# Kernel tuning notes

Measured on AMD Instinct MI355X. Metric: run time of the kernel, lower is better.

Reference implementation:

```python
import jax, jax.numpy as jnp
import numpy as np

N_NODES = 50000
N_EDGES = 1250000
D = 64
EPS = 1e-07


def setup_inputs() -> dict:
    key = jax.random.key(0)
    ks = jax.random.split(key, 10)
    return {
        "node_feats": jax.random.normal(ks[0], (N_NODES, D), jnp.float32),
        "emb0": jax.random.normal(ks[1], (8, D), jnp.float32),
        "emb1": jax.random.normal(ks[2], (4, D), jnp.float32),
        "W": jax.random.normal(ks[3], (D, D), jnp.float32) / np.sqrt(D),
        "b": jnp.zeros((D,), jnp.float32),
        "beta": jnp.ones((1,), jnp.float32),
        "scale": jnp.ones((1,), jnp.float32),
        "src": jax.random.randint(ks[4], (N_EDGES,), 0, N_NODES),
        "dst": jax.random.randint(ks[5], (N_EDGES,), 0, N_NODES),
        "edge_feat0": jax.random.randint(ks[6], (N_EDGES,), 0, 8),
        "edge_feat1": jax.random.randint(ks[7], (N_EDGES,), 0, 4),
    }


def reference(node_feats, emb0, emb1, W, b, beta, scale, src, dst, edge_feat0, edge_feat1):
    n = node_feats.shape[0]
    # edge embeddings summed over categorical feature types
    e = emb0[edge_feat0] + emb1[edge_feat1]              # [E, D]
    # u_add_e then relu + eps
    m = jnp.maximum(node_feats[src] + e, 0.0) + EPS      # [E, D]
    # edge softmax over edges sharing the same destination (per feature dim)
    logits = m * beta                                    # [E, D]
    mx = jax.ops.segment_max(logits, dst, num_segments=n)
    ex = jnp.exp(logits - mx[dst])
    denom = jax.ops.segment_sum(ex, dst, num_segments=n)
    a = ex / denom[dst]                                  # [E, D]
    # scatter-sum aggregation of m * a to destination nodes
    msg = jax.ops.segment_sum(m * a, dst, num_segments=n)  # [N, D]
    # MessageNorm: L2-normalize msg, rescale by ||node_feats|| * scale
    msg_unit = msg / jnp.maximum(
        jnp.linalg.norm(msg, axis=-1, keepdims=True), 1e-12)
    feats_norm = jnp.linalg.norm(node_feats, axis=-1, keepdims=True)
    msg = msg_unit * feats_norm * scale
    # residual + single-layer MLP
    feats = node_feats + msg
    return feats @ W + b
```

## Files before the change

kernel.cpp:

```cpp
#include <hip/hip_runtime.h>

#define NN 50000
#define NE 1250000
#define DD 64
#define KR 391
#define RSH 7
#define RCAP 4096
#define RCSH 12


__global__ __launch_bounds__(512) void k_part(
    const int4* __restrict__ src4, const int4* __restrict__ dst4,
    const int4* __restrict__ ef04, const int4* __restrict__ ef14,
    const float* __restrict__ W, float* __restrict__ Wt,
    int* __restrict__ rcur, unsigned* __restrict__ staging)
{
    __shared__ int hist[KR], rbase[KR], cur[KR];
    const int t  = threadIdx.x;
    const int gb = blockIdx.x;

    for (int i = t; i < KR; i += 512) { hist[i] = 0; cur[i] = 0; }
    if (gb == 0)
        for (int i = t; i < 4096; i += 512)
            Wt[(i & 63) * DD + (i >> 6)] = W[i];
    __syncthreads();

    unsigned pay[8];
    int rr[8];
#pragma unroll
    for (int u = 0; u < 8; ++u) rr[u] = -1;

#pragma unroll
    for (int g = 0; g < 2; ++g) {
        const int i4 = gb * 1024 + t + g * 512;
        if (i4 < NE / 4) {
            const int4 s  = src4[i4], d = dst4[i4];
            const int4 f0 = ef04[i4], f1 = ef14[i4];
            const int ds[4] = {d.x, d.y, d.z, d.w};
            const int ss[4] = {s.x, s.y, s.z, s.w};
            const int a0[4] = {f0.x, f0.y, f0.z, f0.w};
            const int a1[4] = {f1.x, f1.y, f1.z, f1.w};
#pragma unroll
            for (int u = 0; u < 4; ++u) {
                const int k = g * 4 + u;
                rr[k]  = ds[u] >> RSH;
                pay[k] = (unsigned)ss[u] | ((unsigned)(a1[u] * 8 + a0[u]) << 16)
                         | ((unsigned)(ds[u] & 127) << 21);
            }
        }
    }
#pragma unroll
    for (int u = 0; u < 8; ++u)
        if (rr[u] >= 0) atomicAdd(&hist[rr[u]], 1);
    __syncthreads();

    for (int i = t; i < KR; i += 512) {
        const int h = hist[i];
        if (h) rbase[i] = atomicAdd(&rcur[i], h);
    }
    __syncthreads();

#pragma unroll
    for (int u = 0; u < 8; ++u) {
        if (rr[u] >= 0) {
            const int r   = rr[u];
            const int pos = rbase[r] + atomicAdd(&cur[r], 1);
            if (pos < RCAP) staging[(r << RCSH) + pos] = pay[u];
        }
    }
}

__global__ __launch_bounds__(256) void k_bucket(
    const unsigned* __restrict__ staging, const int* __restrict__ rcur,
    int* __restrict__ cnt, unsigned* __restrict__ bucket)
{
    __shared__ unsigned buck[128 * DD];
    __shared__ int ldeg[128];
    const int t = threadIdx.x;
    const int r = blockIdx.x;

    if (t < 128) ldeg[t] = 0;
    __syncthreads();

    const int ne = min(rcur[r], RCAP);
    for (int i = t; i < ne; i += 256) {
        const unsigned p = staging[(r << RCSH) + i];
        const int d = (p >> 21) & 127;
        const int pos = atomicAdd(&ldeg[d], 1);
        if (pos < DD) buck[(d << 6) + pos] = p & 0x1FFFFFu;
    }
    __syncthreads();

    const int base_node = r << RSH;
    const int nnodes = min(128, NN - base_node);
    for (int i = t; i < nnodes * DD; i += 256)
        bucket[((size_t)base_node << 6) + i] = buck[i];
    if (t < nnodes) cnt[base_node + t] = min(ldeg[t], DD);
}

__global__ __launch_bounds__(256, 4) void genconv_agg(
    const float* __restrict__ nf,
    const float* __restrict__ emb0, const float* __restrict__ emb1,
    const float* __restrict__ Wt,  const float* __restrict__ b,
    const float* __restrict__ beta_p, const float* __restrict__ scale_p,
    const int* __restrict__ cnt,
    float* out)
{
    __shared__ float emb_s[32 * DD];
    __shared__ float feat_s[4][DD];

    const int w    = threadIdx.x >> 6;
    const int lane = threadIdx.x & 63;

    for (int i = threadIdx.x; i < 32 * DD; i += 256) {
        const int r = i >> 6, c = i & 63;
        emb_s[i] = emb0[(r & 7) * DD + c] + emb1[(r >> 3) * DD + c];
    }

    float4 wc[16];
#pragma unroll
    for (int k = 0; k < 16; ++k)
        wc[k] = *(const float4*)(Wt + lane * DD + 4 * k);

    const float bias  = b[lane];
    const float beta  = beta_p[0];
    const float scale = scale_p[0];
    __syncthreads();

    const unsigned* bucket = (const unsigned*)out;
    const int stride = gridDim.x * 4;

    int node = blockIdx.x * 4 + w;
    unsigned pl = bucket[(size_t)node * DD + lane];
    int cn = min(cnt[node], DD);

    while (node < NN) {
        const int nnext = node + stride;
        unsigned pl_n = 0u;
        int cn_n = 0;
        if (nnext < NN) {
            pl_n = bucket[(size_t)nnext * DD + lane];
            cn_n = cnt[nnext];
        }
        const float f = nf[(size_t)node * DD + lane];

        float num = 0.0f, den = 0.0f;
        for (int j = 0; j < cn; j += 16) {
            float a[16];
            unsigned qv[16];
#pragma unroll
            for (int u = 0; u < 16; ++u) {
                const unsigned q =
                    (unsigned)__builtin_amdgcn_readlane((int)pl, (j + u) & 63);
                qv[u] = q;
                const int s = min((int)(q & 0xFFFFu), NN - 1);
                a[u] = nf[(size_t)s * DD + lane];
            }
#pragma unroll
            for (int u = 0; u < 16; ++u) {
                const float eb = emb_s[(((qv[u] >> 16) & 31) << 6) + lane];
                const float m  = fmaxf(a[u] + eb, 0.0f) + 1e-7f;
                float x = __expf(beta * m);
                x = (j + u < cn) ? x : 0.0f;
                den += x;
                num = fmaf(m, x, num);
            }
        }

        const float msg = (den > 0.0f) ? num / den : 0.0f;

        float ss = msg * msg;
        float fs = f * f;
#pragma unroll
        for (int m = 32; m >= 1; m >>= 1) {
            ss += __shfl_xor(ss, m, 64);
            fs += __shfl_xor(fs, m, 64);
        }

        const float feat =
            f + msg * (1.0f / fmaxf(sqrtf(ss), 1e-12f)) * sqrtf(fs) * scale;

        feat_s[w][lane] = feat;

        float acc = bias;
#pragma unroll
        for (int k = 0; k < 16; ++k) {
            const float4 fv = *(const float4*)&feat_s[w][4 * k];
            acc = fmaf(fv.x, wc[k].x, acc);
            acc = fmaf(fv.y, wc[k].y, acc);
            acc = fmaf(fv.z, wc[k].z, acc);
            acc = fmaf(fv.w, wc[k].w, acc);
        }
        out[(size_t)node * DD + lane] = acc;

        node = nnext;
        pl = pl_n;
        cn = min(cn_n, DD);
    }
}

extern "C" void kernel_launch(void* const* d_in, const int* in_sizes, int n_in,
                              void* d_out, int out_size, void* d_ws, size_t ws_size,
                              hipStream_t stream)
{
    const float* nf    = (const float*)d_in[0];
    const float* emb0  = (const float*)d_in[1];
    const float* emb1  = (const float*)d_in[2];
    const float* W     = (const float*)d_in[3];
    const float* b     = (const float*)d_in[4];
    const float* beta  = (const float*)d_in[5];
    const float* scale = (const float*)d_in[6];
    const int* src = (const int*)d_in[7];
    const int* dst = (const int*)d_in[8];
    const int* ef0 = (const int*)d_in[9];
    const int* ef1 = (const int*)d_in[10];

    int*      rcur    = (int*)d_ws;
    int*      cnt     = rcur + 512;
    float*    Wt      = (float*)(cnt + 50048);
    unsigned* staging = (unsigned*)(Wt + 4096);

    hipMemsetAsync(rcur, 0, 512 * sizeof(int), stream);

    k_part<<<(NE / 4 + 1023) / 1024, 512, 0, stream>>>(
        (const int4*)src, (const int4*)dst, (const int4*)ef0, (const int4*)ef1,
        W, Wt, rcur, staging);

    k_bucket<<<KR, 256, 0, stream>>>(staging, rcur, cnt, (unsigned*)d_out);

    genconv_agg<<<4096, 256, 0, stream>>>(
        nf, emb0, emb1, Wt, b, beta, scale, cnt, (float*)d_out);
}
```

Measured before the change: 197.8 us.

## Process two edges per wave using half-wave float2 gathers of source features

Each wavefront now splits into two 32-lane halves. Each half gathers a different source edge row as float2, so one load instruction covers two edges and the loop trip count is halved. Partial sums are combined with a lane-32 shuffle, and the norm reductions use fewer shuffle steps. The main loop drops the source-index clamp and the validity masking and adds a separate tail loop. This trades fewer memory instructions and lower loop overhead for the extra cross-half reduction work and the code in the tail loop.

```diff
diff --git a/kernel.cpp b/kernel.cpp
--- a/kernel.cpp
+++ b/kernel.cpp
@@ -106,11 +106,13 @@
     const int* __restrict__ cnt,
     float* out)
 {
-    __shared__ float emb_s[32 * DD];
-    __shared__ float feat_s[4][DD];
+    __shared__ __align__(16) float emb_s[32 * DD];
+    __shared__ __align__(16) float feat_s[4][DD];
 
     const int w    = threadIdx.x >> 6;
     const int lane = threadIdx.x & 63;
+    const int hl   = lane & 31;
+    const int hi   = lane >> 5;
 
     for (int i = threadIdx.x; i < 32 * DD; i += 256) {
         const int r = i >> 6, c = i & 63;
@@ -127,6 +129,8 @@
     const float scale = scale_p[0];
     __syncthreads();
 
+    const float2* __restrict__ nf2  = (const float2*)nf;
+    const float2* __restrict__ emb2 = (const float2*)emb_s;
     const unsigned* bucket = (const unsigned*)out;
     const int stride = gridDim.x * 4;
 
@@ -142,45 +146,85 @@
             pl_n = bucket[(size_t)nnext * DD + lane];
             cn_n = cnt[nnext];
         }
-        const float f = nf[(size_t)node * DD + lane];
-
-        float num = 0.0f, den = 0.0f;
-        for (int j = 0; j < cn; j += 16) {
-            float a[16];
-            unsigned qv[16];
-#pragma unroll
-            for (int u = 0; u < 16; ++u) {
-                const unsigned q =
-                    (unsigned)__builtin_amdgcn_readlane((int)pl, (j + u) & 63);
-                qv[u] = q;
-                const int s = min((int)(q & 0xFFFFu), NN - 1);
-                a[u] = nf[(size_t)s * DD + lane];
-            }
-#pragma unroll
-            for (int u = 0; u < 16; ++u) {
-                const float eb = emb_s[(((qv[u] >> 16) & 31) << 6) + lane];
-                const float m  = fmaxf(a[u] + eb, 0.0f) + 1e-7f;
-                float x = __expf(beta * m);
-                x = (j + u < cn) ? x : 0.0f;
-                den += x;
-                num = fmaf(m, x, num);
-            }
-        }
-
-        const float msg = (den > 0.0f) ? num / den : 0.0f;
-
-        float ss = msg * msg;
-        float fs = f * f;
-#pragma unroll
-        for (int m = 32; m >= 1; m >>= 1) {
+        const float2 f2 = nf2[(node << 5) + hl];
+
+        float2 num2 = make_float2(0.f, 0.f);
+        float2 den2 = make_float2(0.f, 0.f);
+
+        int j = 0;
+        for (; j + 12 <= cn; j += 12) {
+            float2 a2[6];
+            int eo[6];
+#pragma unroll
+            for (int u = 0; u < 6; ++u) {
+                const unsigned qA =
+                    (unsigned)__builtin_amdgcn_readlane((int)pl, j + 2 * u);
+                const unsigned qB =
+                    (unsigned)__builtin_amdgcn_readlane((int)pl, j + 2 * u + 1);
+                const unsigned q = hi ? qB : qA;
+                a2[u] = nf2[((q & 0xFFFFu) << 5) + hl];
+                eo[u] = (int)(q >> 16) << 5;
+            }
+#pragma unroll
+            for (int u = 0; u < 6; ++u) {
+                const float2 e2 = emb2[eo[u] + hl];
+                const float mx = fmaxf(a2[u].x + e2.x, 0.f) + 1e-7f;
+                const float my = fmaxf(a2[u].y + e2.y, 0.f) + 1e-7f;
+                const float xx = __expf(beta * mx);
+                const float xy = __expf(beta * my);
+                den2.x += xx;               den2.y += xy;
+                num2.x = fmaf(mx, xx, num2.x);
+                num2.y = fmaf(my, xy, num2.y);
+            }
+        }
+        if (j < cn) {
+#pragma unroll
+            for (int u = 0; u < 6; ++u) {
+                const unsigned qA =
+                    (unsigned)__builtin_amdgcn_readlane((int)pl, (j + 2 * u) & 63);
+                const unsigned qB =
+                    (unsigned)__builtin_amdgcn_readlane((int)pl, (j + 2 * u + 1) & 63);
+                const unsigned q = hi ? qB : qA;
+                const int row = min((int)(q & 0xFFFFu), NN - 1);
+                const float2 a2 = nf2[(row << 5) + hl];
+                const float2 e2 = emb2[(((q >> 16) & 31) << 5) + hl];
+                const float mx = fmaxf(a2.x + e2.x, 0.f) + 1e-7f;
+                const float my = fmaxf(a2.y + e2.y, 0.f) + 1e-7f;
+                float xx = __expf(beta * mx);
+                float xy = __expf(beta * my);
+                const bool valid = (j + 2 * u + hi) < cn;
+                xx = valid ? xx : 0.f;
+                xy = valid ? xy : 0.f;
+                den2.x += xx;               den2.y += xy;
+                num2.x = fmaf(mx, xx, num2.x);
+                num2.y = fmaf(my, xy, num2.y);
+            }
+        }
+
+        num2.x += __shfl_xor(num2.x, 32, 64);
+        num2.y += __shfl_xor(num2.y, 32, 64);
+        den2.x += __shfl_xor(den2.x, 32, 64);
+        den2.y += __shfl_xor(den2.y, 32, 64);
+
+        float2 msg2;
+        msg2.x = (den2.x > 0.f) ? num2.x / den2.x : 0.f;
+        msg2.y = (den2.y > 0.f) ? num2.y / den2.y : 0.f;
+
+        float ss = msg2.x * msg2.x + msg2.y * msg2.y;
+        float fs = f2.x * f2.x + f2.y * f2.y;
+#pragma unroll
+        for (int m = 16; m >= 1; m >>= 1) {
             ss += __shfl_xor(ss, m, 64);
             fs += __shfl_xor(fs, m, 64);
         }
 
-        const float feat =
-            f + msg * (1.0f / fmaxf(sqrtf(ss), 1e-12f)) * sqrtf(fs) * scale;
-
-        feat_s[w][lane] = feat;
+        const float coef =
+            (1.0f / fmaxf(sqrtf(ss), 1e-12f)) * sqrtf(fs) * scale;
+        float2 feat2;
+        feat2.x = f2.x + msg2.x * coef;
+        feat2.y = f2.y + msg2.y * coef;
+
+        ((float2*)feat_s[w])[hl] = feat2;
 
         float acc = bias;
 #pragma unroll
```

Result: no change. 199.9 us (+1.1%).
